# Performance work log

Hardware: AMD Instinct MI355X
Metric: run time of the kernel (lower is better)

The kernel has to match this reference:

```python
import jax, jax.numpy as jnp
import numpy as np

N_NODES = 100000
D = 64
N_EDGES = 2_000_000
COS_EPS = 1e-6  # nn.CosineSimilarity eps


def setup_inputs() -> dict:
    key = jax.random.key(0)
    k1, k2 = jax.random.split(key)
    node_embs = jax.random.normal(k1, (N_NODES, D), dtype=jnp.float32)
    edge_index = jax.random.randint(k2, (2, N_EDGES), 0, N_NODES, dtype=jnp.int32)
    return {"node_embs": node_embs, "edge_index": edge_index, "temperature": 1}


def reference(node_embs, edge_index, temperature):
    # Edge-wise gather: f1/f2 are [E, D]
    f1 = node_embs[edge_index[0]]
    f2 = node_embs[edge_index[1]]
    # Per-edge cosine similarity (torch semantics: clamp each norm at eps)
    dot = jnp.sum(f1 * f2, axis=1)
    n1 = jnp.maximum(jnp.sqrt(jnp.sum(f1 * f1, axis=1)), COS_EPS)
    n2 = jnp.maximum(jnp.sqrt(jnp.sum(f2 * f2, axis=1)), COS_EPS)
    att_log = dot / (n1 * n2)
    # gumbel_softmax_sample: sigmoid(logits / T), then straight-through threshold
    values = jax.nn.sigmoid(att_log / temperature)
    values_hard = jnp.where(values <= 0.5, jnp.float32(0.0), values)
    out = jax.lax.stop_gradient(values_hard - values) + values
    # out are the sparse graph values (indices = edge_index); att == out
    return out
```

## Files before the change

kernel.cpp:

```cpp
#include <hip/hip_runtime.h>
#include <hip/hip_fp16.h>
#include <math.h>


#define D 64
#define BLOCK 256
#define COS_EPS 1e-6f
#define TAU 6e-3f

#define FMA4(A, X, Y) \
    A.x += X.x * Y.x; A.y += X.y * Y.y; A.z += X.z * Y.z; A.w += X.w * Y.w;

#define PAIRWISE8(E, O) \
    (((E.x + E.y) + (E.z + E.w)) + ((O.x + O.y) + (O.z + O.w)))

typedef _Float16 half2_t __attribute__((ext_vector_type(2)));

__device__ __forceinline__ half2_t as_h2(unsigned u) {
    union { unsigned u; half2_t v; } c; c.u = u; return c.v;
}

__device__ __forceinline__ float dot8_f16(uint4 A, uint4 B, float acc) {
#if __has_builtin(__builtin_amdgcn_fdot2)
    acc = __builtin_amdgcn_fdot2(as_h2(A.x), as_h2(B.x), acc, false);
    acc = __builtin_amdgcn_fdot2(as_h2(A.y), as_h2(B.y), acc, false);
    acc = __builtin_amdgcn_fdot2(as_h2(A.z), as_h2(B.z), acc, false);
    acc = __builtin_amdgcn_fdot2(as_h2(A.w), as_h2(B.w), acc, false);
#else
    const __half2* a = (const __half2*)&A;
    const __half2* b = (const __half2*)&B;
    #pragma unroll
    for (int i = 0; i < 4; ++i) {
        float2 af = __half22float2(a[i]);
        float2 bf = __half22float2(b[i]);
        acc = fmaf(af.x, bf.x, acc);
        acc = fmaf(af.y, bf.y, acc);
    }
#endif
    return acc;
}

__device__ __forceinline__ float read_temperature(const int* temp_ptr) {
    int tbits = *temp_ptr;
    if (tbits >= 1 && tbits < (1 << 23)) return (float)tbits;
    union { int i; float f; } u; u.i = tbits; return u.f;
}

__global__ __launch_bounds__(BLOCK) void quant_kernel(
    const float* __restrict__ in,
    __half*      __restrict__ htab,
    int n_elems)
{
    int t = blockIdx.x * BLOCK + threadIdx.x;
    int base = t * 8;
    if (base >= n_elems) return;
    const float4* p = (const float4*)(in + base);
    float4 a = p[0];
    float4 b = p[1];
    __half2 h[4];
    h[0] = __floats2half2_rn(a.x, a.y);
    h[1] = __floats2half2_rn(a.z, a.w);
    h[2] = __floats2half2_rn(b.x, b.y);
    h[3] = __floats2half2_rn(b.z, b.w);
    *(uint4*)(htab + base) = *(const uint4*)h;
}

__global__ __launch_bounds__(BLOCK) void node_norm_kernel(
    const float* __restrict__ node_embs,
    float*       __restrict__ dnorm,
    int n_nodes)
{
    int n = blockIdx.x * BLOCK + threadIdx.x;
    if (n >= n_nodes) return;

    const float4* __restrict__ r = (const float4*)(node_embs + (size_t)n * D);
    float4 z = make_float4(0.f, 0.f, 0.f, 0.f);
    float4 aE = z, aO = z;
    #pragma unroll
    for (int k = 0; k < D / 4; k += 2) {
        float4 x0 = r[k];
        float4 x1 = r[k + 1];
        FMA4(aE, x0, x0)
        FMA4(aO, x1, x1)
    }
    float s = PAIRWISE8(aE, aO);
    dnorm[n] = fmaxf(sqrtf(s), COS_EPS);
}

__global__ __launch_bounds__(BLOCK) void GraphLearner_68513318306086_kernel(
    const float* __restrict__ node_embs,
    const __half* __restrict__ htab,
    const int*   __restrict__ edge_index,
    const float* __restrict__ dnorm,
    const int*   __restrict__ temp_ptr,
    float*       __restrict__ out,
    int n_edges)
{
    int t    = blockIdx.x * BLOCK + threadIdx.x;
    int e    = t >> 3;
    int lane = threadIdx.x & 7;
    if (e >= n_edges) return;

    int i0 = edge_index[e];
    int i1 = edge_index[n_edges + e];

    const uint4* __restrict__ rA = (const uint4*)(htab + i0 * D);
    const uint4* __restrict__ rB = (const uint4*)(htab + i1 * D);
    uint4 A = rA[lane];
    uint4 B = rB[lane];

    float p = dot8_f16(A, B, 0.0f);

    #pragma unroll
    for (int m = 1; m < 8; m <<= 1) p += __shfl_xor(p, m, 8);

    float d1 = dnorm[i0];
    float d2 = dnorm[i1];
    float inv = 1.0f / (d1 * d2);
    float cosv = p * inv;

    if (fabsf(cosv) < TAU) {
        const float4* __restrict__ r0 = (const float4*)(node_embs + (size_t)i0 * D);
        const float4* __restrict__ r1 = (const float4*)(node_embs + (size_t)i1 * D);
        float4 x0 = r0[lane];
        float4 x1 = r0[lane + 8];
        float4 y0 = r1[lane];
        float4 y1 = r1[lane + 8];
        float pp = ((x0.x * y0.x + x0.y * y0.y) + (x0.z * y0.z + x0.w * y0.w))
                 + ((x1.x * y1.x + x1.y * y1.y) + (x1.z * y1.z + x1.w * y1.w));
        #pragma unroll
        for (int m = 1; m < 8; m <<= 1) pp += __shfl_xor(pp, m, 8);
        cosv = pp / (d1 * d2);
    }

    if (lane == 0) {
        float T = read_temperature(temp_ptr);
        float v = 1.0f / (1.0f + expf(-(cosv / T)));
        out[e] = (v <= 0.5f) ? 0.0f : v;
    }
}

__global__ __launch_bounds__(BLOCK) void edge_kernel_fused(
    const float* __restrict__ node_embs,
    const int*   __restrict__ edge_index,
    const int*   __restrict__ temp_ptr,
    float*       __restrict__ out,
    int n_edges)
{
    int t    = blockIdx.x * BLOCK + threadIdx.x;
    int e    = t >> 3;
    int lane = threadIdx.x & 7;
    if (e >= n_edges) return;

    int i0 = edge_index[e];
    int i1 = edge_index[n_edges + e];

    const float4* __restrict__ r0 = (const float4*)(node_embs + (size_t)i0 * D);
    const float4* __restrict__ r1 = (const float4*)(node_embs + (size_t)i1 * D);

    float4 x0 = r0[lane];
    float4 x1 = r0[lane + 8];
    float4 y0 = r1[lane];
    float4 y1 = r1[lane + 8];

    float p  = ((x0.x * y0.x + x0.y * y0.y) + (x0.z * y0.z + x0.w * y0.w))
             + ((x1.x * y1.x + x1.y * y1.y) + (x1.z * y1.z + x1.w * y1.w));
    float a  = ((x0.x * x0.x + x0.y * x0.y) + (x0.z * x0.z + x0.w * x0.w))
             + ((x1.x * x1.x + x1.y * x1.y) + (x1.z * x1.z + x1.w * x1.w));
    float b  = ((y0.x * y0.x + y0.y * y0.y) + (y0.z * y0.z + y0.w * y0.w))
             + ((y1.x * y1.x + y1.y * y1.y) + (y1.z * y1.z + y1.w * y1.w));

    #pragma unroll
    for (int m = 1; m < 8; m <<= 1) {
        p += __shfl_xor(p, m, 8);
        a += __shfl_xor(a, m, 8);
        b += __shfl_xor(b, m, 8);
    }

    if (lane == 0) {
        float T    = read_temperature(temp_ptr);
        float d1   = fmaxf(sqrtf(a), COS_EPS);
        float d2   = fmaxf(sqrtf(b), COS_EPS);
        float cosv = p / (d1 * d2);
        float v    = 1.0f / (1.0f + expf(-(cosv / T)));
        out[e] = (v <= 0.5f) ? 0.0f : v;
    }
}

extern "C" void kernel_launch(void* const* d_in, const int* in_sizes, int n_in,
                              void* d_out, int out_size, void* d_ws, size_t ws_size,
                              hipStream_t stream) {
    const float* node_embs  = (const float*)d_in[0];
    const int*   edge_index = (const int*)d_in[1];
    const int*   temp_ptr   = (const int*)d_in[2];
    float*       out        = (float*)d_out;

    int n_nodes = in_sizes[0] / D;
    int n_elems = in_sizes[0];
    int n_edges = in_sizes[1] / 2;

    size_t htab_bytes = (size_t)n_elems * sizeof(__half);
    size_t need = htab_bytes + (size_t)n_nodes * sizeof(float);

    long long edge_threads = (long long)n_edges * 8;
    int grid_e = (int)((edge_threads + BLOCK - 1) / BLOCK);

    if (ws_size >= need) {
        __half* htab = (__half*)d_ws;
        float*  dnorm = (float*)((char*)d_ws + htab_bytes);

        int grid_q = (n_elems / 8 + BLOCK - 1) / BLOCK;
        quant_kernel<<<grid_q, BLOCK, 0, stream>>>(node_embs, htab, n_elems);

        int grid_n = (n_nodes + BLOCK - 1) / BLOCK;
        node_norm_kernel<<<grid_n, BLOCK, 0, stream>>>(node_embs, dnorm, n_nodes);

        GraphLearner_68513318306086_kernel<<<grid_e, BLOCK, 0, stream>>>(
            node_embs, htab, edge_index, dnorm, temp_ptr, out, n_edges);
    } else {
        edge_kernel_fused<<<grid_e, BLOCK, 0, stream>>>(
            node_embs, edge_index, temp_ptr, out, n_edges);
    }
}
```

Baseline: 156.0 us.

## Pre-normalize fp16 node table so edge kernel skips norm gathers

Node rows are now divided by their clamped norm before fp16 quantization, so the edge dot product directly yields the cosine and the per-edge gathers of two norm values disappear from the common path. The quant kernel is reordered after the norm kernel and reads dnorm. Row addressing is simplified to a uint4 index, and the sigmoid uses hardware rcp/exp2 intrinsics with the threshold tested on the logit sign. The risk is fp16 rounding of normalized values near the TAU fallback boundary, plus slightly different rounding from the approximate intrinsics.

```diff
diff --git a/kernel.cpp b/kernel.cpp
--- a/kernel.cpp
+++ b/kernel.cpp
@@ -7,6 +7,7 @@
 #define BLOCK 256
 #define COS_EPS 1e-6f
 #define TAU 6e-3f
+#define LOG2E 1.4426950408889634f
 
 #define FMA4(A, X, Y) \
     A.x += X.x * Y.x; A.y += X.y * Y.y; A.z += X.z * Y.z; A.w += X.w * Y.w;
@@ -46,25 +47,6 @@
     union { int i; float f; } u; u.i = tbits; return u.f;
 }
 
-__global__ __launch_bounds__(BLOCK) void quant_kernel(
-    const float* __restrict__ in,
-    __half*      __restrict__ htab,
-    int n_elems)
-{
-    int t = blockIdx.x * BLOCK + threadIdx.x;
-    int base = t * 8;
-    if (base >= n_elems) return;
-    const float4* p = (const float4*)(in + base);
-    float4 a = p[0];
-    float4 b = p[1];
-    __half2 h[4];
-    h[0] = __floats2half2_rn(a.x, a.y);
-    h[1] = __floats2half2_rn(a.z, a.w);
-    h[2] = __floats2half2_rn(b.x, b.y);
-    h[3] = __floats2half2_rn(b.z, b.w);
-    *(uint4*)(htab + base) = *(const uint4*)h;
-}
-
 __global__ __launch_bounds__(BLOCK) void node_norm_kernel(
     const float* __restrict__ node_embs,
     float*       __restrict__ dnorm,
@@ -85,6 +67,27 @@
     }
     float s = PAIRWISE8(aE, aO);
     dnorm[n] = fmaxf(sqrtf(s), COS_EPS);
+}
+
+__global__ __launch_bounds__(BLOCK) void normquant_kernel(
+    const float* __restrict__ in,
+    const float* __restrict__ dnorm,
+    __half*      __restrict__ htab,
+    int n_elems)
+{
+    int t = blockIdx.x * BLOCK + threadIdx.x;
+    int base = t * 8;
+    if (base >= n_elems) return;
+    float inv = 1.0f / dnorm[t >> 3];
+    const float4* p = (const float4*)(in + base);
+    float4 a = p[0];
+    float4 b = p[1];
+    __half2 h[4];
+    h[0] = __floats2half2_rn(a.x * inv, a.y * inv);
+    h[1] = __floats2half2_rn(a.z * inv, a.w * inv);
+    h[2] = __floats2half2_rn(b.x * inv, b.y * inv);
+    h[3] = __floats2half2_rn(b.z * inv, b.w * inv);
+    *(uint4*)(htab + base) = *(const uint4*)h;
 }
 
 __global__ __launch_bounds__(BLOCK) void GraphLearner_68513318306086_kernel(
@@ -104,21 +107,16 @@
     int i0 = edge_index[e];
     int i1 = edge_index[n_edges + e];
 
-    const uint4* __restrict__ rA = (const uint4*)(htab + i0 * D);
-    const uint4* __restrict__ rB = (const uint4*)(htab + i1 * D);
-    uint4 A = rA[lane];
-    uint4 B = rB[lane];
+    const uint4* __restrict__ tab = (const uint4*)htab;
+    uint4 A = tab[(i0 << 3) + lane];
+    uint4 B = tab[(i1 << 3) + lane];
 
     float p = dot8_f16(A, B, 0.0f);
 
     #pragma unroll
     for (int m = 1; m < 8; m <<= 1) p += __shfl_xor(p, m, 8);
 
-    float d1 = dnorm[i0];
-    float d2 = dnorm[i1];
-    float inv = 1.0f / (d1 * d2);
-    float cosv = p * inv;
-
+    float cosv = p;
     if (fabsf(cosv) < TAU) {
         const float4* __restrict__ r0 = (const float4*)(node_embs + (size_t)i0 * D);
         const float4* __restrict__ r1 = (const float4*)(node_embs + (size_t)i1 * D);
@@ -130,13 +128,16 @@
                  + ((x1.x * y1.x + x1.y * y1.y) + (x1.z * y1.z + x1.w * y1.w));
         #pragma unroll
         for (int m = 1; m < 8; m <<= 1) pp += __shfl_xor(pp, m, 8);
-        cosv = pp / (d1 * d2);
+        cosv = pp / (dnorm[i0] * dnorm[i1]);
     }
 
     if (lane == 0) {
-        float T = read_temperature(temp_ptr);
-        float v = 1.0f / (1.0f + expf(-(cosv / T)));
-        out[e] = (v <= 0.5f) ? 0.0f : v;
+        float T    = read_temperature(temp_ptr);
+        float invT = __builtin_amdgcn_rcpf(T);
+        float x    = cosv * invT;
+        float ex   = __builtin_amdgcn_exp2f(-x * LOG2E);
+        float v    = __builtin_amdgcn_rcpf(1.0f + ex);
+        out[e] = (x <= 0.0f) ? 0.0f : v;
     }
 }
 
@@ -206,14 +207,14 @@
     int grid_e = (int)((edge_threads + BLOCK - 1) / BLOCK);
 
     if (ws_size >= need) {
-        __half* htab = (__half*)d_ws;
+        __half* htab  = (__half*)d_ws;
         float*  dnorm = (float*)((char*)d_ws + htab_bytes);
-
-        int grid_q = (n_elems / 8 + BLOCK - 1) / BLOCK;
-        quant_kernel<<<grid_q, BLOCK, 0, stream>>>(node_embs, htab, n_elems);
 
         int grid_n = (n_nodes + BLOCK - 1) / BLOCK;
         node_norm_kernel<<<grid_n, BLOCK, 0, stream>>>(node_embs, dnorm, n_nodes);
+
+        int grid_q = (n_elems / 8 + BLOCK - 1) / BLOCK;
+        normquant_kernel<<<grid_q, BLOCK, 0, stream>>>(node_embs, dnorm, htab, n_elems);
 
         GraphLearner_68513318306086_kernel<<<grid_e, BLOCK, 0, stream>>>(
             node_embs, htab, edge_index, dnorm, temp_ptr, out, n_edges);
```

New measurement: 153.1 us. Within noise of the previous version (-1.8%).
